# Performance work log

Hardware: AMD Instinct MI355X
Metric: run time of the kernel (lower is better)

Reference implementation:

```python
import jax, jax.numpy as jnp
import numpy as np

B, L, D, H = 4, 2048, 1024, 16
DH = D // H  # 64
MASK_VALUE = -1000000.0
EPS = 1e-12


def setup_inputs() -> dict:
    key = jax.random.key(0)
    ks = jax.random.split(key, 7)
    s = 1.0 / np.sqrt(D)
    x = jax.random.normal(ks[0], (B, L, D), dtype=jnp.float32)
    Wq = jax.random.uniform(ks[1], (D, H * DH), jnp.float32, -s, s)
    Wk = jax.random.uniform(ks[2], (D, H * DH), jnp.float32, -s, s)
    Wv = jax.random.uniform(ks[3], (D, H * DH), jnp.float32, -s, s)
    Wo = jax.random.uniform(ks[4], (H * DH, D), jnp.float32, -s, s)
    gamma = jnp.ones((D,), jnp.float32)
    beta = jnp.zeros((D,), jnp.float32)
    # causal mask: True positions are masked (query m cannot attend to key n > m)
    attn_mask = jnp.triu(jnp.ones((L, L), dtype=bool), k=1)
    return {"x": x, "Wq": Wq, "Wk": Wk, "Wv": Wv, "Wo": Wo,
            "gamma": gamma, "beta": beta, "attn_mask": attn_mask}


def _layernorm(y, gamma, beta):
    mu = jnp.mean(y, axis=-1, keepdims=True)
    var = jnp.mean(jnp.square(y - mu), axis=-1, keepdims=True)
    return (y - mu) * jax.lax.rsqrt(var + EPS) * gamma + beta


def reference(x, Wq, Wk, Wv, Wo, gamma, beta, attn_mask):
    scale = 1.0 / np.sqrt(DH)
    # projections, reshape to heads: B L (H D) -> B H L D
    q = (x @ Wq).reshape(B, L, H, DH).transpose(0, 2, 1, 3)
    k = (x @ Wk).reshape(B, L, H, DH).transpose(0, 2, 1, 3)
    v = (x @ Wv).reshape(B, L, H, DH).transpose(0, 2, 1, 3)
    scores = jnp.einsum('bhmd,bhnd->bhmn', q, k) * scale
    scores = jnp.where(attn_mask, MASK_VALUE, scores)
    probs = jax.nn.softmax(scores, axis=-1)
    z = jnp.einsum('bhmn,bhnd->bhmd', probs, v)
    z = z.transpose(0, 2, 1, 3).reshape(B, L, H * DH)
    out = jax.nn.relu(z @ Wo)
    return _layernorm(out + x, gamma, beta)
```

## Files before the change

### kernel.cpp

```cpp
#include <hip/hip_runtime.h>
#include <math.h>

#define B_ 4
#define L_ 2048
#define D_ 1024
#define H_ 16
#define DH_ 64
#define QKV_N 3072

typedef unsigned short ushort_t;
typedef unsigned int uint_t;
using bf16x8 = __attribute__((ext_vector_type(8))) short;
using f32x4  = __attribute__((ext_vector_type(4))) float;

__device__ __forceinline__ ushort_t f2bf(float f) {
    union { float f; unsigned int u; } v; v.f = f;
    unsigned int u = v.u;
    unsigned int rnd = ((u >> 16) & 1u) + 0x7fffu;
    return (ushort_t)((u + rnd) >> 16);
}

__device__ __forceinline__ void glds16(const void* g, void* l) {
    __builtin_amdgcn_global_load_lds(
        (const __attribute__((address_space(1))) unsigned int*)g,
        (__attribute__((address_space(3))) unsigned int*)l, 16, 0, 0);
}

__global__ __launch_bounds__(256) void prep(const float* __restrict__ Wq,
                                            const float* __restrict__ Wk,
                                            const float* __restrict__ Wv,
                                            const float* __restrict__ Wo,
                                            const float* __restrict__ x,
                                            ushort_t* __restrict__ wcat,
                                            ushort_t* __restrict__ wto,
                                            ushort_t* __restrict__ xb) {
    const int t = threadIdx.x;
    if (blockIdx.z == 4) {
        const int bid = blockIdx.y * 16 + blockIdx.x;
        const int base = bid * 32768 + t * 4;
        #pragma unroll
        for (int it = 0; it < 32; ++it) {
            float4 v = *(const float4*)(x + base + it * 1024);
            ushort4 o;
            o.x = f2bf(v.x); o.y = f2bf(v.y); o.z = f2bf(v.z); o.w = f2bf(v.w);
            *(ushort4*)(xb + base + it * 1024) = o;
        }
        return;
    }
    __shared__ ushort_t tile[64][65];
    const int widx = blockIdx.z;
    const float* W = (widx == 0) ? Wq : (widx == 1) ? Wk : (widx == 2) ? Wv : Wo;
    ushort_t* dst = (widx < 3) ? (wcat + (size_t)widx * 1024 * 1024) : wto;
    const int j = t & 63, i0 = t >> 6;
    const int kbase = blockIdx.y * 64, nbase = blockIdx.x * 64;
    #pragma unroll
    for (int it = 0; it < 16; ++it) {
        int i = it * 4 + i0;
        tile[i][j] = f2bf(W[(size_t)(kbase + i) * 1024 + nbase + j]);
    }
    __syncthreads();
    #pragma unroll
    for (int it = 0; it < 16; ++it) {
        int nn = it * 4 + i0;
        dst[(size_t)(nbase + nn) * 1024 + kbase + j] = tile[j][nn];
    }
}

__global__ __launch_bounds__(256) void gemm_mfma(const ushort_t* __restrict__ A,
                                                 const ushort_t* __restrict__ Wt,
                                                 ushort_t* __restrict__ Cbf,
                                                 float* __restrict__ Cf,
                                                 const float* __restrict__ resid,
                                                 int M, int N, int K, int fuse) {
    __shared__ ushort_t As[128 * 32];
    __shared__ ushort_t Bs[128 * 32];
    const int t = threadIdx.x;
    const int w = t >> 6, ln = t & 63;
    const int l15 = ln & 15, quad = ln >> 4;
    const int bm = blockIdx.y * 128, bn = blockIdx.x * 128;
    const int wm = (w & 1) * 64, wn = (w >> 1) * 64;

    const int r0 = t >> 2;
    const int r1 = (t + 256) >> 2;
    const int qp = t & 3;
    const int qg0 = qp ^ ((r0 >> 1) & 3);
    const int qg1 = qp ^ ((r1 >> 1) & 3);

    const ushort_t* Ap0 = A + (size_t)(bm + r0) * K + qg0 * 8;
    const ushort_t* Ap1 = A + (size_t)(bm + r1) * K + qg1 * 8;
    const ushort_t* Bp0 = Wt + (size_t)(bn + r0) * K + qg0 * 8;
    const ushort_t* Bp1 = Wt + (size_t)(bn + r1) * K + qg1 * 8;
    ushort_t* As0 = &As[t * 8];
    ushort_t* As1 = &As[(t + 256) * 8];
    ushort_t* Bs0 = &Bs[t * 8];
    ushort_t* Bs1 = &Bs[(t + 256) * 8];

    f32x4 acc[4][4] = {};

    for (int k0 = 0; k0 < K; k0 += 32) {
        __syncthreads();
        glds16(Ap0 + k0, As0);
        glds16(Ap1 + k0, As1);
        glds16(Bp0 + k0, Bs0);
        glds16(Bp1 + k0, Bs1);
        __syncthreads();

        bf16x8 af[4], bfr[4];
        #pragma unroll
        for (int im = 0; im < 4; ++im) {
            int row = wm + im * 16 + l15;
            int phys = quad ^ ((row >> 1) & 3);
            af[im] = *(const bf16x8*)&As[row * 32 + phys * 8];
        }
        #pragma unroll
        for (int in = 0; in < 4; ++in) {
            int row = wn + in * 16 + l15;
            int phys = quad ^ ((row >> 1) & 3);
            bfr[in] = *(const bf16x8*)&Bs[row * 32 + phys * 8];
        }
        #pragma unroll
        for (int im = 0; im < 4; ++im)
            #pragma unroll
            for (int in = 0; in < 4; ++in)
                acc[im][in] = __builtin_amdgcn_mfma_f32_16x16x32_bf16(
                    bfr[in], af[im], acc[im][in], 0, 0, 0);
    }

    if (fuse) {
        #pragma unroll
        for (int im = 0; im < 4; ++im) {
            const int m = bm + wm + im * 16 + l15;
            #pragma unroll
            for (int in = 0; in < 4; ++in) {
                const int nb = bn + wn + in * 16 + quad * 4;
                const size_t idx = (size_t)m * N + nb;
                float4 res = *(const float4*)(resid + idx);
                f32x4 a = acc[im][in];
                float4 o;
                o.x = fmaxf(a[0], 0.f) + res.x;
                o.y = fmaxf(a[1], 0.f) + res.y;
                o.z = fmaxf(a[2], 0.f) + res.z;
                o.w = fmaxf(a[3], 0.f) + res.w;
                *(float4*)(Cf + idx) = o;
            }
        }
    } else {
        #pragma unroll
        for (int im = 0; im < 4; ++im) {
            const int m = bm + wm + im * 16 + l15;
            #pragma unroll
            for (int in = 0; in < 4; ++in) {
                const int nb = bn + wn + in * 16 + quad * 4;
                f32x4 a = acc[im][in];
                ushort4 o;
                o.x = f2bf(a[0]); o.y = f2bf(a[1]);
                o.z = f2bf(a[2]); o.w = f2bf(a[3]);
                *(ushort4*)(Cbf + (size_t)m * N + nb) = o;
            }
        }
    }
}

__global__ __launch_bounds__(256) void transv(const ushort_t* __restrict__ qkv,
                                              ushort_t* __restrict__ Vt) {
    __shared__ ushort_t tile[64][65];
    const int t = threadIdx.x, j = t & 63, i0 = t >> 6;
    const int tt = blockIdx.x, h = blockIdx.y, b = blockIdx.z;
    #pragma unroll
    for (int it = 0; it < 16; ++it) {
        int i = it * 4 + i0;
        tile[i][j] = qkv[(size_t)(b * L_ + tt * 64 + i) * QKV_N + 2048 + h * DH_ + j];
    }
    __syncthreads();
    const int pj = (j & 3) * 16 + (j >> 2);
    #pragma unroll
    for (int it = 0; it < 16; ++it) {
        int d = it * 4 + i0;
        Vt[(size_t)((b * H_ + h) * DH_ + d) * L_ + tt * 64 + j] = tile[pj][d];
    }
}

__global__ __launch_bounds__(256) void attn_mfma(const ushort_t* __restrict__ qkv,
                                                 const ushort_t* __restrict__ Vt,
                                                 ushort_t* __restrict__ Zb) {
    __shared__ ushort_t Ks[128 * 64];
    __shared__ ushort_t Vs[64 * 128];
    __shared__ ushort_t Ps[4][32 * 72];
    const int t = threadIdx.x, w = t >> 6, ln = t & 63;
    const int l15 = ln & 15, quad = ln >> 4;
    const int bh = blockIdx.x;
    const int b = bh >> 4, h = bh & 15;
    const int Qt = 15 - blockIdx.y;

    bf16x8 ones;
    #pragma unroll
    for (int i = 0; i < 8; ++i) ones[i] = (short)0x3f80;

    int kkey[4], kq[4], vd[4], vcq[4];
    #pragma unroll
    for (int j = 0; j < 4; ++j) {
        int i = t + j * 256;
        kkey[j] = i >> 3;
        kq[j]   = (i & 7) ^ (kkey[j] & 7);
        vd[j]   = i >> 4;
        int cqp = i & 15;
        vcq[j]  = (cqp & 8) | ((cqp & 7) ^ (vd[j] & 7));
    }
    const ushort_t* Kgb = qkv + 1024 + (size_t)b * L_ * QKV_N + h * DH_;
    const ushort_t* Vgb = Vt + (size_t)((b * H_ + h) * DH_) * L_;

    bf16x8 qf[2][2];
    #pragma unroll
    for (int mt = 0; mt < 2; ++mt) {
        const ushort_t* qrow =
            qkv + (size_t)(b * L_ + Qt * 128 + w * 32 + mt * 16 + l15) * QKV_N + h * DH_;
        qf[mt][0] = *(const bf16x8*)(qrow + quad * 8);
        qf[mt][1] = *(const bf16x8*)(qrow + 32 + quad * 8);
    }

    f32x4 acc_o[2][4] = {};
    f32x4 l_acc[2] = {};

    const float c2 = 0.18033688f;

    for (int kt = 0; kt <= Qt; ++kt) {
        __syncthreads();
        #pragma unroll
        for (int j = 0; j < 4; ++j) {
            glds16(Kgb + (size_t)(kt * 128 + kkey[j]) * QKV_N + kq[j] * 8,
                   &Ks[(t + j * 256) * 8]);
            glds16(Vgb + (size_t)vd[j] * L_ + kt * 128 + vcq[j] * 8,
                   &Vs[(t + j * 256) * 8]);
        }
        __syncthreads();

        const bool masked = (kt == Qt);

        #pragma unroll
        for (int ph = 0; ph < 2; ++ph) {
            if (masked && ph && w < 2) continue;

            f32x4 acc_s[2][4] = {};
            #pragma unroll
            for (int in = 0; in < 4; ++in) {
                const int key = ph * 64 + in * 16 + l15;
                #pragma unroll
                for (int ks = 0; ks < 2; ++ks) {
                    int phys = (ks * 4 + quad) ^ (key & 7);
                    bf16x8 kf = *(const bf16x8*)&Ks[key * 64 + phys * 8];
                    acc_s[0][in] = __builtin_amdgcn_mfma_f32_16x16x32_bf16(
                        qf[0][ks], kf, acc_s[0][in], 0, 0, 0);
                    acc_s[1][in] = __builtin_amdgcn_mfma_f32_16x16x32_bf16(
                        qf[1][ks], kf, acc_s[1][in], 0, 0, 0);
                }
            }

            #pragma unroll
            for (int mt = 0; mt < 2; ++mt) {
                #pragma unroll
                for (int reg = 0; reg < 4; ++reg) {
                    const int row = mt * 16 + quad * 4 + reg;
                    float pv[4];
                    #pragma unroll
                    for (int in = 0; in < 4; ++in) {
                        float s2 = fmaf(acc_s[mt][in][reg], c2, -2.0f);
                        if (masked) {
                            int col = kt * 128 + ph * 64 + in * 16 + l15;
                            int qg  = Qt * 128 + w * 32 + row;
                            s2 = (col > qg) ? -100000.0f : s2;
                        }
                        pv[in] = __builtin_amdgcn_exp2f(s2);
                    }
                    uint_t u01 = __builtin_amdgcn_perm(
                        __float_as_uint(pv[1]), __float_as_uint(pv[0]), 0x07060302u);
                    uint_t u23 = __builtin_amdgcn_perm(
                        __float_as_uint(pv[3]), __float_as_uint(pv[2]), 0x07060302u);
                    uint2* dst = (uint2*)&Ps[w][row * 72 + l15 * 4];
                    *dst = make_uint2(u01, u23);
                }
            }

            #pragma unroll
            for (int ks = 0; ks < 2; ++ks) {
                bf16x8 pf0 = *(const bf16x8*)&Ps[w][(l15) * 72 + ks * 32 + quad * 8];
                bf16x8 pf1 = *(const bf16x8*)&Ps[w][(16 + l15) * 72 + ks * 32 + quad * 8];
                #pragma unroll
                for (int in = 0; in < 4; ++in) {
                    const int d = in * 16 + l15;
                    int physv = ph * 8 + (((ks * 4 + quad) ^ (d & 7)));
                    bf16x8 vf = *(const bf16x8*)&Vs[d * 128 + physv * 8];
                    acc_o[0][in] = __builtin_amdgcn_mfma_f32_16x16x32_bf16(
                        vf, pf0, acc_o[0][in], 0, 0, 0);
                    acc_o[1][in] = __builtin_amdgcn_mfma_f32_16x16x32_bf16(
                        vf, pf1, acc_o[1][in], 0, 0, 0);
                }
                l_acc[0] = __builtin_amdgcn_mfma_f32_16x16x32_bf16(ones, pf0, l_acc[0], 0, 0, 0);
                l_acc[1] = __builtin_amdgcn_mfma_f32_16x16x32_bf16(ones, pf1, l_acc[1], 0, 0, 0);
            }
        }
    }

    #pragma unroll
    for (int mt = 0; mt < 2; ++mt) {
        const float inv = 1.0f / l_acc[mt][0];
        const int row = b * L_ + Qt * 128 + w * 32 + mt * 16 + l15;
        #pragma unroll
        for (int in = 0; in < 4; ++in) {
            const int dbase = h * DH_ + in * 16 + quad * 4;
            f32x4 a = acc_o[mt][in];
            ushort4 o;
            o.x = f2bf(a[0] * inv); o.y = f2bf(a[1] * inv);
            o.z = f2bf(a[2] * inv); o.w = f2bf(a[3] * inv);
            *(ushort4*)(Zb + (size_t)row * D_ + dbase) = o;
        }
    }
}

__global__ __launch_bounds__(256) void ln_kernel(const float* __restrict__ Y,
                                                 const float* __restrict__ gamma,
                                                 const float* __restrict__ beta,
                                                 float* __restrict__ out) {
    const int row = blockIdx.x;
    const int t = threadIdx.x;
    const float* y = Y + (size_t)row * D_;

    float4 v = *(const float4*)(y + t * 4);
    __shared__ float red[256];

    float s = v.x + v.y + v.z + v.w;
    red[t] = s;
    __syncthreads();
    for (int st = 128; st > 0; st >>= 1) {
        if (t < st) red[t] += red[t + st];
        __syncthreads();
    }
    const float mu = red[0] * (1.f / (float)D_);
    __syncthreads();

    const float dx = v.x - mu, dy = v.y - mu, dz = v.z - mu, dw = v.w - mu;
    s = dx * dx + dy * dy + dz * dz + dw * dw;
    red[t] = s;
    __syncthreads();
    for (int st = 128; st > 0; st >>= 1) {
        if (t < st) red[t] += red[t + st];
        __syncthreads();
    }
    const float var = red[0] * (1.f / (float)D_);
    const float rstd = rsqrtf(var + 1e-12f);

    float4 g  = *(const float4*)(gamma + t * 4);
    float4 bb = *(const float4*)(beta + t * 4);
    float4 o;
    o.x = dx * rstd * g.x + bb.x;
    o.y = dy * rstd * g.y + bb.y;
    o.z = dz * rstd * g.z + bb.z;
    o.w = dw * rstd * g.w + bb.w;
    *(float4*)(out + (size_t)row * D_ + t * 4) = o;
}

extern "C" void kernel_launch(void* const* d_in, const int* in_sizes, int n_in,
                              void* d_out, int out_size, void* d_ws, size_t ws_size,
                              hipStream_t stream) {
    const float* x     = (const float*)d_in[0];
    const float* Wq    = (const float*)d_in[1];
    const float* Wk    = (const float*)d_in[2];
    const float* Wv    = (const float*)d_in[3];
    const float* Wo    = (const float*)d_in[4];
    const float* gamma = (const float*)d_in[5];
    const float* beta  = (const float*)d_in[6];
    float* out = (float*)d_out;

    char* ws = (char*)d_ws;
    ushort_t* x_bf = (ushort_t*)(ws);
    ushort_t* wcat = (ushort_t*)(ws + (16u  << 20));
    ushort_t* wto  = (ushort_t*)(ws + (22u  << 20));
    ushort_t* qkv  = (ushort_t*)(ws + (24u  << 20));
    ushort_t* vt   = (ushort_t*)(ws + (72u  << 20));
    ushort_t* z_bf = (ushort_t*)(ws + (88u  << 20));
    float*    y    = (float*)   (ws + (104u << 20));

    const int M = B_ * L_;

    prep<<<dim3(16, 16, 5), 256, 0, stream>>>(Wq, Wk, Wv, Wo, x, wcat, wto, x_bf);

    gemm_mfma<<<dim3(QKV_N / 128, M / 128), 256, 0, stream>>>(
        x_bf, wcat, qkv, nullptr, nullptr, M, QKV_N, D_, 0);

    transv<<<dim3(L_ / 64, H_, B_), 256, 0, stream>>>(qkv, vt);

    attn_mfma<<<dim3(B_ * H_, 16), 256, 0, stream>>>(qkv, vt, z_bf);

    gemm_mfma<<<dim3(D_ / 128, M / 128), 256, 0, stream>>>(
        z_bf, wto, nullptr, y, x, M, D_, D_, 1);

    ln_kernel<<<M, 256, 0, stream>>>(y, gamma, beta, out);
}
```

Baseline: 313.0 us.

## Deepen GEMM K-tile, store bf16 intermediates, use a single-wave shuffle layernorm

```diff
diff --git a/kernel.cpp b/kernel.cpp
--- a/kernel.cpp
+++ b/kernel.cpp
@@ -18,6 +18,12 @@
     unsigned int u = v.u;
     unsigned int rnd = ((u >> 16) & 1u) + 0x7fffu;
     return (ushort_t)((u + rnd) >> 16);
+}
+
+__device__ __forceinline__ float bf2f(ushort_t u) {
+    union { unsigned int u; float f; } v;
+    v.u = ((unsigned int)u) << 16;
+    return v.f;
 }
 
 __device__ __forceinline__ void glds16(const void* g, void* l) {
@@ -69,93 +75,74 @@
 __global__ __launch_bounds__(256) void gemm_mfma(const ushort_t* __restrict__ A,
                                                  const ushort_t* __restrict__ Wt,
                                                  ushort_t* __restrict__ Cbf,
-                                                 float* __restrict__ Cf,
-                                                 const float* __restrict__ resid,
+                                                 const ushort_t* __restrict__ resid,
                                                  int M, int N, int K, int fuse) {
-    __shared__ ushort_t As[128 * 32];
-    __shared__ ushort_t Bs[128 * 32];
+    __shared__ ushort_t As[128 * 64];
+    __shared__ ushort_t Bs[128 * 64];
     const int t = threadIdx.x;
     const int w = t >> 6, ln = t & 63;
     const int l15 = ln & 15, quad = ln >> 4;
     const int bm = blockIdx.y * 128, bn = blockIdx.x * 128;
     const int wm = (w & 1) * 64, wn = (w >> 1) * 64;
 
-    const int r0 = t >> 2;
-    const int r1 = (t + 256) >> 2;
-    const int qp = t & 3;
-    const int qg0 = qp ^ ((r0 >> 1) & 3);
-    const int qg1 = qp ^ ((r1 >> 1) & 3);
-
-    const ushort_t* Ap0 = A + (size_t)(bm + r0) * K + qg0 * 8;
-    const ushort_t* Ap1 = A + (size_t)(bm + r1) * K + qg1 * 8;
-    const ushort_t* Bp0 = Wt + (size_t)(bn + r0) * K + qg0 * 8;
-    const ushort_t* Bp1 = Wt + (size_t)(bn + r1) * K + qg1 * 8;
-    ushort_t* As0 = &As[t * 8];
-    ushort_t* As1 = &As[(t + 256) * 8];
-    ushort_t* Bs0 = &Bs[t * 8];
-    ushort_t* Bs1 = &Bs[(t + 256) * 8];
+    const ushort_t* Ap[4];
+    const ushort_t* Bp[4];
+    #pragma unroll
+    for (int j = 0; j < 4; ++j) {
+        const int i = t + j * 256;
+        const int r = i >> 3;
+        const int qg = (i & 7) ^ (r & 7);
+        Ap[j] = A  + (size_t)(bm + r) * K + qg * 8;
+        Bp[j] = Wt + (size_t)(bn + r) * K + qg * 8;
+    }
 
     f32x4 acc[4][4] = {};
 
-    for (int k0 = 0; k0 < K; k0 += 32) {
+    for (int k0 = 0; k0 < K; k0 += 64) {
         __syncthreads();
-        glds16(Ap0 + k0, As0);
-        glds16(Ap1 + k0, As1);
-        glds16(Bp0 + k0, Bs0);
-        glds16(Bp1 + k0, Bs1);
+        #pragma unroll
+        for (int j = 0; j < 4; ++j) {
+            glds16(Ap[j] + k0, &As[(t + j * 256) * 8]);
+            glds16(Bp[j] + k0, &Bs[(t + j * 256) * 8]);
+        }
         __syncthreads();
 
-        bf16x8 af[4], bfr[4];
-        #pragma unroll
-        for (int im = 0; im < 4; ++im) {
-            int row = wm + im * 16 + l15;
-            int phys = quad ^ ((row >> 1) & 3);
-            af[im] = *(const bf16x8*)&As[row * 32 + phys * 8];
-        }
+        #pragma unroll
+        for (int kw = 0; kw < 2; ++kw) {
+            bf16x8 af[4], bfr[4];
+            #pragma unroll
+            for (int im = 0; im < 4; ++im) {
+                int row = wm + im * 16 + l15;
+                int phys = (kw * 4 + quad) ^ (row & 7);
+                af[im] = *(const bf16x8*)&As[row * 64 + phys * 8];
+            }
+            #pragma unroll
+            for (int in = 0; in < 4; ++in) {
+                int row = wn + in * 16 + l15;
+                int phys = (kw * 4 + quad) ^ (row & 7);
+                bfr[in] = *(const bf16x8*)&Bs[row * 64 + phys * 8];
+            }
+            #pragma unroll
+            for (int im = 0; im < 4; ++im)
+                #pragma unroll
+                for (int in = 0; in < 4; ++in)
+                    acc[im][in] = __builtin_amdgcn_mfma_f32_16x16x32_bf16(
+                        af[im], bfr[in], acc[im][in], 0, 0, 0);
+        }
+    }
+
+    #pragma unroll
+    for (int im = 0; im < 4; ++im) {
         #pragma unroll
         for (int in = 0; in < 4; ++in) {
-            int row = wn + in * 16 + l15;
-            int phys = quad ^ ((row >> 1) & 3);
-            bfr[in] = *(const bf16x8*)&Bs[row * 32 + phys * 8];
-        }
-        #pragma unroll
-        for (int im = 0; im < 4; ++im)
-            #pragma unroll
-            for (int in = 0; in < 4; ++in)
-                acc[im][in] = __builtin_amdgcn_mfma_f32_16x16x32_bf16(
-                    bfr[in], af[im], acc[im][in], 0, 0, 0);
-    }
-
-    if (fuse) {
-        #pragma unroll
-        for (int im = 0; im < 4; ++im) {
-            const int m = bm + wm + im * 16 + l15;
-            #pragma unroll
-            for (int in = 0; in < 4; ++in) {
-                const int nb = bn + wn + in * 16 + quad * 4;
-                const size_t idx = (size_t)m * N + nb;
-                float4 res = *(const float4*)(resid + idx);
-                f32x4 a = acc[im][in];
-                float4 o;
-                o.x = fmaxf(a[0], 0.f) + res.x;
-                o.y = fmaxf(a[1], 0.f) + res.y;
-                o.z = fmaxf(a[2], 0.f) + res.z;
-                o.w = fmaxf(a[3], 0.f) + res.w;
-                *(float4*)(Cf + idx) = o;
-            }
-        }
-    } else {
-        #pragma unroll
-        for (int im = 0; im < 4; ++im) {
-            const int m = bm + wm + im * 16 + l15;
-            #pragma unroll
-            for (int in = 0; in < 4; ++in) {
-                const int nb = bn + wn + in * 16 + quad * 4;
-                f32x4 a = acc[im][in];
-                ushort4 o;
-                o.x = f2bf(a[0]); o.y = f2bf(a[1]);
-                o.z = f2bf(a[2]); o.w = f2bf(a[3]);
-                *(ushort4*)(Cbf + (size_t)m * N + nb) = o;
+            #pragma unroll
+            for (int reg = 0; reg < 4; ++reg) {
+                int row = bm + wm + im * 16 + quad * 4 + reg;
+                int col = bn + wn + in * 16 + l15;
+                size_t idx = (size_t)row * N + col;
+                float v = acc[im][in][reg];
+                if (fuse) v = fmaxf(v, 0.f) + bf2f(resid[idx]);
+                Cbf[idx] = f2bf(v);
             }
         }
     }
@@ -316,46 +303,53 @@
     }
 }
 
-__global__ __launch_bounds__(256) void ln_kernel(const float* __restrict__ Y,
-                                                 const float* __restrict__ gamma,
-                                                 const float* __restrict__ beta,
-                                                 float* __restrict__ out) {
+__global__ __launch_bounds__(64) void ln_kernel(const ushort_t* __restrict__ Y,
+                                                const float* __restrict__ gamma,
+                                                const float* __restrict__ beta,
+                                                float* __restrict__ out) {
     const int row = blockIdx.x;
     const int t = threadIdx.x;
-    const float* y = Y + (size_t)row * D_;
-
-    float4 v = *(const float4*)(y + t * 4);
-    __shared__ float red[256];
-
-    float s = v.x + v.y + v.z + v.w;
-    red[t] = s;
-    __syncthreads();
-    for (int st = 128; st > 0; st >>= 1) {
-        if (t < st) red[t] += red[t + st];
-        __syncthreads();
-    }
-    const float mu = red[0] * (1.f / (float)D_);
-    __syncthreads();
-
-    const float dx = v.x - mu, dy = v.y - mu, dz = v.z - mu, dw = v.w - mu;
-    s = dx * dx + dy * dy + dz * dz + dw * dw;
-    red[t] = s;
-    __syncthreads();
-    for (int st = 128; st > 0; st >>= 1) {
-        if (t < st) red[t] += red[t + st];
-        __syncthreads();
-    }
-    const float var = red[0] * (1.f / (float)D_);
-    const float rstd = rsqrtf(var + 1e-12f);
-
-    float4 g  = *(const float4*)(gamma + t * 4);
-    float4 bb = *(const float4*)(beta + t * 4);
-    float4 o;
-    o.x = dx * rstd * g.x + bb.x;
-    o.y = dy * rstd * g.y + bb.y;
-    o.z = dz * rstd * g.z + bb.z;
-    o.w = dw * rstd * g.w + bb.w;
-    *(float4*)(out + (size_t)row * D_ + t * 4) = o;
+    const ushort_t* y = Y + (size_t)row * D_;
+
+    float v[16];
+    #pragma unroll
+    for (int s = 0; s < 4; ++s) {
+        ushort4 u = *(const ushort4*)(y + s * 256 + t * 4);
+        v[s * 4 + 0] = bf2f(u.x);
+        v[s * 4 + 1] = bf2f(u.y);
+        v[s * 4 + 2] = bf2f(u.z);
+        v[s * 4 + 3] = bf2f(u.w);
+    }
+
+    float sum = 0.f;
+    #pragma unroll
+    for (int i = 0; i < 16; ++i) sum += v[i];
+    #pragma unroll
+    for (int k = 1; k < 64; k <<= 1) sum += __shfl_xor(sum, k, 64);
+    const float mu = sum * (1.f / (float)D_);
+
+    float var = 0.f;
+    #pragma unroll
+    for (int i = 0; i < 16; ++i) {
+        float d = v[i] - mu;
+        var += d * d;
+    }
+    #pragma unroll
+    for (int k = 1; k < 64; k <<= 1) var += __shfl_xor(var, k, 64);
+    const float rstd = rsqrtf(var * (1.f / (float)D_) + 1e-12f);
+
+    #pragma unroll
+    for (int s = 0; s < 4; ++s) {
+        const int col = s * 256 + t * 4;
+        float4 g  = *(const float4*)(gamma + col);
+        float4 bb = *(const float4*)(beta + col);
+        float4 o;
+        o.x = (v[s * 4 + 0] - mu) * rstd * g.x + bb.x;
+        o.y = (v[s * 4 + 1] - mu) * rstd * g.y + bb.y;
+        o.z = (v[s * 4 + 2] - mu) * rstd * g.z + bb.z;
+        o.w = (v[s * 4 + 3] - mu) * rstd * g.w + bb.w;
+        *(float4*)(out + (size_t)row * D_ + col) = o;
+    }
 }
 
 extern "C" void kernel_launch(void* const* d_in, const int* in_sizes, int n_in,
@@ -377,21 +371,21 @@
     ushort_t* qkv  = (ushort_t*)(ws + (24u  << 20));
     ushort_t* vt   = (ushort_t*)(ws + (72u  << 20));
     ushort_t* z_bf = (ushort_t*)(ws + (88u  << 20));
-    float*    y    = (float*)   (ws + (104u << 20));
+    ushort_t* y_bf = (ushort_t*)(ws + (104u << 20));
 
     const int M = B_ * L_;
 
     prep<<<dim3(16, 16, 5), 256, 0, stream>>>(Wq, Wk, Wv, Wo, x, wcat, wto, x_bf);
 
     gemm_mfma<<<dim3(QKV_N / 128, M / 128), 256, 0, stream>>>(
-        x_bf, wcat, qkv, nullptr, nullptr, M, QKV_N, D_, 0);
+        x_bf, wcat, qkv, nullptr, M, QKV_N, D_, 0);
 
     transv<<<dim3(L_ / 64, H_, B_), 256, 0, stream>>>(qkv, vt);
 
     attn_mfma<<<dim3(B_ * H_, 16), 256, 0, stream>>>(qkv, vt, z_bf);
 
     gemm_mfma<<<dim3(D_ / 128, M / 128), 256, 0, stream>>>(
-        z_bf, wto, nullptr, y, x, M, D_, D_, 1);
-
-    ln_kernel<<<M, 256, 0, stream>>>(y, gamma, beta, out);
-}
+        z_bf, wto, y_bf, x_bf, M, D_, D_, 1);
+
+    ln_kernel<<<M, 64, 0, stream>>>(y_bf, gamma, beta, out);
+}
```

Result: faster. 288.3 us (-7.9%).
